# Kernel tuning notes

Measured on AMD Instinct MI355X. Metric: run time of the kernel, lower is better.

## Reference

```python
import jax, jax.numpy as jnp
import numpy as np

B, S, C, HD = 2, 4096, 2048, 128
H = C // HD  # 16 heads
EPS = 1.1920929e-07  # torch RMSNorm default eps for float32 (finfo.eps)


def _make_rope(seq_len, head_dim):
    # Standard RoPE 2x2 rotation matrices: [1, S, 1, head_dim//2, 2, 2]
    half = head_dim // 2
    freqs = 1.0 / (10000.0 ** (np.arange(0, half, dtype=np.float32) / half))
    ang = np.arange(seq_len, dtype=np.float32)[:, None] * freqs[None, :]  # [S, half]
    cos, sin = np.cos(ang), np.sin(ang)
    rot = np.stack([np.stack([cos, -sin], axis=-1),
                    np.stack([sin, cos], axis=-1)], axis=-2)  # [S, half, 2, 2]
    return jnp.asarray(rot[None, :, None])  # [1, S, 1, half, 2, 2]


def setup_inputs() -> dict:
    key = jax.random.key(0)
    ks = jax.random.split(key, 9)
    sc = 1.0 / np.sqrt(C)
    return {
        "x": jax.random.normal(ks[0], (B, S, C), jnp.float32),
        "rope": _make_rope(S, HD),
        "wq": jax.random.normal(ks[1], (C, C), jnp.float32) * sc,
        "bq": jax.random.normal(ks[2], (C,), jnp.float32) * 0.01,
        "wk": jax.random.normal(ks[3], (C, C), jnp.float32) * sc,
        "bk": jax.random.normal(ks[4], (C,), jnp.float32) * 0.01,
        "wv": jax.random.normal(ks[5], (C, C), jnp.float32) * sc,
        "bv": jax.random.normal(ks[6], (C,), jnp.float32) * 0.01,
        "q_norm_w": jnp.ones((HD,), jnp.float32),
        "k_norm_w": jnp.ones((HD,), jnp.float32),
    }


def _rmsnorm(t, w):
    t32 = t.astype(jnp.float32)
    inv = jax.lax.rsqrt(jnp.mean(t32 * t32, axis=-1, keepdims=True) + EPS)
    return (t32 * inv * w).astype(t.dtype)


def _apply_rotary(t, rope):
    # t: [B, S, H, HD] -> pairs [B, S, H, HD//2, 1, 2]; rope: [1, S, 1, HD//2, 2, 2]
    t32 = t.reshape(*t.shape[:-1], HD // 2, 1, 2).astype(jnp.float32)
    out = (rope * t32).sum(axis=-1)  # [B, S, H, HD//2, 2]
    return out.reshape(t.shape).astype(t.dtype)


def reference(x, rope, wq, bq, wk, bk, wv, bv, q_norm_w, k_norm_w):
    # QKV projections (torch Linear: x @ W^T + b)
    q = (jnp.einsum('bsc,oc->bso', x, wq) + bq).reshape(B, S, H, HD)
    k = (jnp.einsum('bsc,oc->bso', x, wk) + bk).reshape(B, S, H, HD)
    v = (jnp.einsum('bsc,oc->bso', x, wv) + bv).reshape(B, S, H, HD)
    # Per-head RMSNorm on q, k (in float32, cast back), then rotary
    q = _apply_rotary(_rmsnorm(q, q_norm_w), rope)
    k = _apply_rotary(_rmsnorm(k, k_norm_w), rope)
    return (q, k, v)
```

## Files before the change

kernel.cpp:

```cpp
#include <hip/hip_runtime.h>


#define M_DIM 8192
#define N_DIM 6144
#define K_DIM 2048
#define NKT 32
#define EPS_RMS 1.1920929e-07f

typedef __bf16 bf16x8 __attribute__((ext_vector_type(8)));
typedef float f32x4 __attribute__((ext_vector_type(4)));

__device__ __forceinline__ void gload16(const void* g, void* l) {
  __builtin_amdgcn_global_load_lds(
      (const __attribute__((address_space(1))) unsigned int*)g,
      (__attribute__((address_space(3))) unsigned int*)l, 16, 0, 0);
}

__device__ __forceinline__ unsigned short f2bf(float f) {
  union { float f; unsigned u; } x; x.f = f;
  unsigned r = x.u + 0x7FFFu + ((x.u >> 16) & 1u);
  return (unsigned short)(r >> 16);
}

__global__ void __launch_bounds__(256) cvt_kernel(const float* __restrict__ s,
                                                  unsigned short* __restrict__ d, int n4) {
  int i = blockIdx.x * blockDim.x + threadIdx.x;
  const int stride = gridDim.x * blockDim.x;
  for (; i < n4; i += stride) {
    const float4 v = reinterpret_cast<const float4*>(s)[i];
    ushort4 o;
    o.x = f2bf(v.x); o.y = f2bf(v.y); o.z = f2bf(v.z); o.w = f2bf(v.w);
    reinterpret_cast<ushort4*>(d)[i] = o;
  }
}

#define LDS4(ARR, BASE, OFF) (*(const f32x4*)((const char*)(ARR) + (BASE) + (OFF)))

#define MFMA_PH(MH, NH)                                                              \
  {                                                                                  \
    _Pragma("unroll")                                                                \
    for (int mf4 = 0; mf4 < 4; ++mf4) {                                              \
      _Pragma("unroll")                                                              \
      for (int nf2 = 0; nf2 < 2; ++nf2) {                                            \
        f32x4& c = acc[(MH) * 4 + mf4][(NH) * 2 + nf2];                              \
        c = __builtin_amdgcn_mfma_f32_16x16x32_bf16(                                 \
            __builtin_bit_cast(bf16x8, Af[mf4][0]),                                  \
            __builtin_bit_cast(bf16x8, Bf[NH][nf2][0]), c, 0, 0, 0);                 \
        c = __builtin_amdgcn_mfma_f32_16x16x32_bf16(                                 \
            __builtin_bit_cast(bf16x8, Af[mf4][1]),                                  \
            __builtin_bit_cast(bf16x8, Bf[NH][nf2][1]), c, 0, 0, 0);                 \
      }                                                                              \
    }                                                                                \
  }

__global__ void __launch_bounds__(512, 2) gemm_fused(
    const unsigned short* __restrict__ xbf, const unsigned short* __restrict__ wbf,
    const float* __restrict__ rope,
    const float* __restrict__ bq, const float* __restrict__ bk, const float* __restrict__ bv,
    const float* __restrict__ qnw, const float* __restrict__ knw,
    float* __restrict__ dout) {
  const int id = blockIdx.x;
  const int sw = (id & 7) * 96 + (id >> 3);
  const int bm = sw / 24;
  const int bn = sw - bm * 24;
  const int m0 = bm << 8, n0 = bn << 8;
  const int tid = threadIdx.x;
  const int w = tid >> 6, l = tid & 63;
  const int l15 = l & 15, lhi = l >> 4;
  const int wr = w >> 2, wc = w & 3;

  __shared__ __align__(16) unsigned short As[32768];
  __shared__ __align__(16) unsigned short Bs[32768];

  const int srow = tid >> 3;
  const int schunk = (tid & 7) ^ (srow & 7);
  const unsigned short* aSrc = xbf + ((size_t)(m0 + srow) << 11) + (schunk << 3);
  const unsigned short* bSrc = wbf + ((size_t)(n0 + srow) << 11) + (schunk << 3);
  char* aDst = (char*)As + (w << 10);
  char* bDst = (char*)Bs + (w << 10);

#define STA(KT, Q) gload16(aSrc + ((size_t)(Q) << 17) + ((KT) << 6), aDst + ((((KT) & 1) << 15) + ((Q) << 13)))
#define STB(KT, Q) gload16(bSrc + ((size_t)(Q) << 17) + ((KT) << 6), bDst + ((((KT) & 1) << 15) + ((Q) << 13)))

  const int sl0 = ((lhi ^ (l15 & 7)) << 4);
  const int sl1 = (((lhi + 4) ^ (l15 & 7)) << 4);
  unsigned a0 = (wr << 14) + (l15 << 7) + sl0;
  unsigned a1 = (wr << 14) + (l15 << 7) + sl1;
  unsigned b0 = (wc << 13) + (l15 << 7) + sl0;
  unsigned b1 = (wc << 13) + (l15 << 7) + sl1;

  f32x4 acc[8][4];
#pragma unroll
  for (int i = 0; i < 8; ++i)
#pragma unroll
    for (int j = 0; j < 4; ++j) acc[i][j] = (f32x4){0.f, 0.f, 0.f, 0.f};

  f32x4 Af[4][2];
  f32x4 Bf[2][2][2];

  STA(0, 0); STA(0, 2);
  STB(0, 0); STB(0, 1); STB(0, 2); STB(0, 3);
  STA(0, 1); STA(0, 3);
  asm volatile("s_waitcnt vmcnt(2)" ::: "memory");
  __builtin_amdgcn_s_barrier();
  asm volatile("" ::: "memory");

  for (int kt = 0; kt < NKT; ++kt) {
    const bool notLast = (kt < NKT - 1);
    Af[0][0] = LDS4(As, a0, 0);    Af[1][0] = LDS4(As, a0, 2048);
    Af[2][0] = LDS4(As, a0, 4096); Af[3][0] = LDS4(As, a0, 6144);
    Af[0][1] = LDS4(As, a1, 0);    Af[1][1] = LDS4(As, a1, 2048);
    Af[2][1] = LDS4(As, a1, 4096); Af[3][1] = LDS4(As, a1, 6144);
    Bf[0][0][0] = LDS4(Bs, b0, 0);    Bf[0][1][0] = LDS4(Bs, b0, 2048);
    Bf[0][0][1] = LDS4(Bs, b1, 0);    Bf[0][1][1] = LDS4(Bs, b1, 2048);
    Bf[1][0][0] = LDS4(Bs, b0, 4096); Bf[1][1][0] = LDS4(Bs, b0, 6144);
    Bf[1][0][1] = LDS4(Bs, b1, 4096); Bf[1][1][1] = LDS4(Bs, b1, 6144);
    if (notLast) {
      STA(kt + 1, 0); STA(kt + 1, 2);
      STB(kt + 1, 0); STB(kt + 1, 1); STB(kt + 1, 2); STB(kt + 1, 3);
    }
    __builtin_amdgcn_s_setprio(1);
    MFMA_PH(0, 0);
    MFMA_PH(0, 1);
    __builtin_amdgcn_s_setprio(0);
    if (notLast) { asm volatile("s_waitcnt vmcnt(6)" ::: "memory"); }
    else         { asm volatile("s_waitcnt vmcnt(0)" ::: "memory"); }
    __builtin_amdgcn_s_barrier();
    asm volatile("" ::: "memory");
    Af[0][0] = LDS4(As, a0, 8192);  Af[1][0] = LDS4(As, a0, 10240);
    Af[2][0] = LDS4(As, a0, 12288); Af[3][0] = LDS4(As, a0, 14336);
    Af[0][1] = LDS4(As, a1, 8192);  Af[1][1] = LDS4(As, a1, 10240);
    Af[2][1] = LDS4(As, a1, 12288); Af[3][1] = LDS4(As, a1, 14336);
    if (notLast) { STA(kt + 1, 1); STA(kt + 1, 3); }
    __builtin_amdgcn_s_setprio(1);
    MFMA_PH(1, 0);
    MFMA_PH(1, 1);
    __builtin_amdgcn_s_setprio(0);
    if (notLast) { asm volatile("s_waitcnt vmcnt(2)" ::: "memory"); }
    __builtin_amdgcn_s_barrier();
    asm volatile("" ::: "memory");
    a0 ^= 32768u; a1 ^= 32768u; b0 ^= 32768u; b1 ^= 32768u;
  }

  float* scr = (float*)As;
  const int sec = bn >> 3;
  const int nsec = (n0 & 2047) + (wc << 6);
  const float* bias = sec == 0 ? bq : (sec == 1 ? bk : bv);
  float biasv[4];
#pragma unroll
  for (int nf = 0; nf < 4; ++nf) biasv[nf] = bias[nsec + nf * 16 + l15];
  const size_t outBase = ((size_t)sec << 24);

  if (sec < 2) {
    const float* nwp = sec ? knw : qnw;
    const int colh = (wc & 1) << 6;
    float nwv[4];
#pragma unroll
    for (int nf = 0; nf < 4; ++nf) nwv[nf] = nwp[colh + nf * 16 + l15];
    float ssv[8][4];
#pragma unroll
    for (int mf = 0; mf < 8; ++mf) {
#pragma unroll
      for (int j = 0; j < 4; ++j) {
        float ss = 0.f;
#pragma unroll
        for (int nf = 0; nf < 4; ++nf) {
          const float t = acc[mf][nf][j] + biasv[nf];
          ss += t * t;
        }
        ss += __shfl_xor(ss, 1);
        ss += __shfl_xor(ss, 2);
        ss += __shfl_xor(ss, 4);
        ss += __shfl_xor(ss, 8);
        ssv[mf][j] = ss;
      }
    }
    if (l15 == 0) {
#pragma unroll
      for (int mf = 0; mf < 8; ++mf)
#pragma unroll
        for (int j = 0; j < 4; ++j)
          scr[(w << 7) + mf * 16 + (lhi << 2) + j] = ssv[mf][j];
    }
    __syncthreads();
#pragma unroll
    for (int mf = 0; mf < 8; ++mf) {
#pragma unroll
      for (int j = 0; j < 4; ++j) {
        const float tot = ssv[mf][j] + scr[((w ^ 1) << 7) + mf * 16 + (lhi << 2) + j];
        const float inv = rsqrtf(tot * (1.0f / 128.0f) + EPS_RMS);
        const int m = m0 + (wr << 7) + mf * 16 + (lhi << 2) + j;
        const float* rp = rope + ((size_t)(m & 4095) << 8);
        float* orow = dout + outBase + ((size_t)m << 11) + nsec + l15;
#pragma unroll
        for (int nf = 0; nf < 4; ++nf) {
          const float tn = (acc[mf][nf][j] + biasv[nf]) * inv * nwv[nf];
          const float pn = __shfl_xor(tn, 1);
          const int ch = colh + nf * 16 + l15;
          const int jr = ch >> 1;
          const float o = fmaf(rp[jr << 2], tn, rp[(jr << 2) + 1 + (ch & 1)] * pn);
          orow[nf << 4] = o;
        }
      }
    }
  } else {
#pragma unroll
    for (int mf = 0; mf < 8; ++mf)
#pragma unroll
      for (int j = 0; j < 4; ++j) {
        const int m = m0 + (wr << 7) + mf * 16 + (lhi << 2) + j;
        float* orow = dout + outBase + ((size_t)m << 11) + nsec + l15;
#pragma unroll
        for (int nf = 0; nf < 4; ++nf) orow[nf << 4] = acc[mf][nf][j] + biasv[nf];
      }
  }
}

extern "C" void kernel_launch(void* const* d_in, const int* in_sizes, int n_in,
                              void* d_out, int out_size, void* d_ws, size_t ws_size,
                              hipStream_t stream) {
  const float* x = (const float*)d_in[0];
  const float* rope = (const float*)d_in[1];
  const float* wq = (const float*)d_in[2];
  const float* bq = (const float*)d_in[3];
  const float* wk = (const float*)d_in[4];
  const float* bk = (const float*)d_in[5];
  const float* wv = (const float*)d_in[6];
  const float* bv = (const float*)d_in[7];
  const float* qnw = (const float*)d_in[8];
  const float* knw = (const float*)d_in[9];

  unsigned short* xbf = (unsigned short*)d_ws;
  unsigned short* wbf = xbf + (size_t)M_DIM * K_DIM;

  cvt_kernel<<<2048, 256, 0, stream>>>(x, xbf, M_DIM * K_DIM / 4);
  cvt_kernel<<<1024, 256, 0, stream>>>(wq, wbf, K_DIM * K_DIM / 4);
  cvt_kernel<<<1024, 256, 0, stream>>>(wk, wbf + (size_t)K_DIM * K_DIM, K_DIM * K_DIM / 4);
  cvt_kernel<<<1024, 256, 0, stream>>>(wv, wbf + (size_t)2 * K_DIM * K_DIM, K_DIM * K_DIM / 4);

  gemm_fused<<<(M_DIM / 256) * (N_DIM / 256), 512, 0, stream>>>(
      xbf, wbf, rope, bq, bk, bv, qnw, knw, (float*)d_out);
}
```

Baseline: 261.2 us.

## Interleave LDS reads with MFMAs via sched_group_barrier and remap tile order per XCD

Reorders the LDS fragment loads so the operands for the first MFMAs arrive first, and adds sched_group_barrier hints that interleave ds_read groups with MFMA groups in both half-iterations. This is meant to hide LDS latency behind matrix math instead of issuing every read up front. It also changes the block-to-tile mapping so each XCD owns 4 contiguous M-tiles across all N-tiles, which changes L2 reuse patterns. The scheduling constraints could raise register pressure or serialize issue if the group counts do not match the real instruction stream.

```diff
diff --git a/kernel.cpp b/kernel.cpp
--- a/kernel.cpp
+++ b/kernel.cpp
@@ -35,6 +35,9 @@
 }
 
 #define LDS4(ARR, BASE, OFF) (*(const f32x4*)((const char*)(ARR) + (BASE) + (OFF)))
+
+#define SGB_DS(N)   __builtin_amdgcn_sched_group_barrier(0x100, (N), 0)
+#define SGB_MFMA(N) __builtin_amdgcn_sched_group_barrier(0x8, (N), 0)
 
 #define MFMA_PH(MH, NH)                                                              \
   {                                                                                  \
@@ -60,9 +63,10 @@
     const float* __restrict__ qnw, const float* __restrict__ knw,
     float* __restrict__ dout) {
   const int id = blockIdx.x;
-  const int sw = (id & 7) * 96 + (id >> 3);
-  const int bm = sw / 24;
-  const int bn = sw - bm * 24;
+  const int xcd = id & 7;
+  const int j = id >> 3;
+  const int bm = (xcd << 2) | (j & 3);
+  const int bn = j >> 2;
   const int m0 = bm << 8, n0 = bn << 8;
   const int tid = threadIdx.x;
   const int w = tid >> 6, l = tid & 63;
@@ -93,7 +97,7 @@
 #pragma unroll
   for (int i = 0; i < 8; ++i)
 #pragma unroll
-    for (int j = 0; j < 4; ++j) acc[i][j] = (f32x4){0.f, 0.f, 0.f, 0.f};
+    for (int jj = 0; jj < 4; ++jj) acc[i][jj] = (f32x4){0.f, 0.f, 0.f, 0.f};
 
   f32x4 Af[4][2];
   f32x4 Bf[2][2][2];
@@ -107,14 +111,14 @@
 
   for (int kt = 0; kt < NKT; ++kt) {
     const bool notLast = (kt < NKT - 1);
-    Af[0][0] = LDS4(As, a0, 0);    Af[1][0] = LDS4(As, a0, 2048);
-    Af[2][0] = LDS4(As, a0, 4096); Af[3][0] = LDS4(As, a0, 6144);
-    Af[0][1] = LDS4(As, a1, 0);    Af[1][1] = LDS4(As, a1, 2048);
-    Af[2][1] = LDS4(As, a1, 4096); Af[3][1] = LDS4(As, a1, 6144);
-    Bf[0][0][0] = LDS4(Bs, b0, 0);    Bf[0][1][0] = LDS4(Bs, b0, 2048);
-    Bf[0][0][1] = LDS4(Bs, b1, 0);    Bf[0][1][1] = LDS4(Bs, b1, 2048);
-    Bf[1][0][0] = LDS4(Bs, b0, 4096); Bf[1][1][0] = LDS4(Bs, b0, 6144);
-    Bf[1][0][1] = LDS4(Bs, b1, 4096); Bf[1][1][1] = LDS4(Bs, b1, 6144);
+    Af[0][0] = LDS4(As, a0, 0);        Af[0][1] = LDS4(As, a1, 0);
+    Bf[0][0][0] = LDS4(Bs, b0, 0);     Bf[0][0][1] = LDS4(Bs, b1, 0);
+    Bf[0][1][0] = LDS4(Bs, b0, 2048);  Bf[0][1][1] = LDS4(Bs, b1, 2048);
+    Af[1][0] = LDS4(As, a0, 2048);     Af[1][1] = LDS4(As, a1, 2048);
+    Af[2][0] = LDS4(As, a0, 4096);     Af[2][1] = LDS4(As, a1, 4096);
+    Af[3][0] = LDS4(As, a0, 6144);     Af[3][1] = LDS4(As, a1, 6144);
+    Bf[1][0][0] = LDS4(Bs, b0, 4096);  Bf[1][0][1] = LDS4(Bs, b1, 4096);
+    Bf[1][1][0] = LDS4(Bs, b0, 6144);  Bf[1][1][1] = LDS4(Bs, b1, 6144);
     if (notLast) {
       STA(kt + 1, 0); STA(kt + 1, 2);
       STB(kt + 1, 0); STB(kt + 1, 1); STB(kt + 1, 2); STB(kt + 1, 3);
@@ -122,19 +126,30 @@
     __builtin_amdgcn_s_setprio(1);
     MFMA_PH(0, 0);
     MFMA_PH(0, 1);
+    SGB_DS(4);  SGB_MFMA(2);
+    SGB_DS(2);  SGB_MFMA(2);
+    SGB_DS(2);  SGB_MFMA(4);
+    SGB_DS(2);  SGB_MFMA(4);
+    SGB_DS(2);  SGB_MFMA(4);
+    SGB_DS(4);  SGB_MFMA(16);
     __builtin_amdgcn_s_setprio(0);
     if (notLast) { asm volatile("s_waitcnt vmcnt(6)" ::: "memory"); }
     else         { asm volatile("s_waitcnt vmcnt(0)" ::: "memory"); }
     __builtin_amdgcn_s_barrier();
     asm volatile("" ::: "memory");
-    Af[0][0] = LDS4(As, a0, 8192);  Af[1][0] = LDS4(As, a0, 10240);
-    Af[2][0] = LDS4(As, a0, 12288); Af[3][0] = LDS4(As, a0, 14336);
-    Af[0][1] = LDS4(As, a1, 8192);  Af[1][1] = LDS4(As, a1, 10240);
-    Af[2][1] = LDS4(As, a1, 12288); Af[3][1] = LDS4(As, a1, 14336);
+    Af[0][0] = LDS4(As, a0, 8192);  Af[0][1] = LDS4(As, a1, 8192);
+    Af[1][0] = LDS4(As, a0, 10240); Af[1][1] = LDS4(As, a1, 10240);
+    Af[2][0] = LDS4(As, a0, 12288); Af[2][1] = LDS4(As, a1, 12288);
+    Af[3][0] = LDS4(As, a0, 14336); Af[3][1] = LDS4(As, a1, 14336);
     if (notLast) { STA(kt + 1, 1); STA(kt + 1, 3); }
     __builtin_amdgcn_s_setprio(1);
     MFMA_PH(1, 0);
     MFMA_PH(1, 1);
+    SGB_DS(2);  SGB_MFMA(4);
+    SGB_DS(2);  SGB_MFMA(4);
+    SGB_DS(2);  SGB_MFMA(4);
+    SGB_DS(2);  SGB_MFMA(4);
+    SGB_MFMA(16);
     __builtin_amdgcn_s_setprio(0);
     if (notLast) { asm volatile("s_waitcnt vmcnt(2)" ::: "memory"); }
     __builtin_amdgcn_s_barrier();
@@ -161,40 +176,40 @@
 #pragma unroll
     for (int mf = 0; mf < 8; ++mf) {
 #pragma unroll
-      for (int j = 0; j < 4; ++j) {
+      for (int jj = 0; jj < 4; ++jj) {
         float ss = 0.f;
 #pragma unroll
         for (int nf = 0; nf < 4; ++nf) {
-          const float t = acc[mf][nf][j] + biasv[nf];
+          const float t = acc[mf][nf][jj] + biasv[nf];
           ss += t * t;
         }
         ss += __shfl_xor(ss, 1);
         ss += __shfl_xor(ss, 2);
         ss += __shfl_xor(ss, 4);
         ss += __shfl_xor(ss, 8);
-        ssv[mf][j] = ss;
+        ssv[mf][jj] = ss;
       }
     }
     if (l15 == 0) {
 #pragma unroll
       for (int mf = 0; mf < 8; ++mf)
 #pragma unroll
-        for (int j = 0; j < 4; ++j)
-          scr[(w << 7) + mf * 16 + (lhi << 2) + j] = ssv[mf][j];
+        for (int jj = 0; jj < 4; ++jj)
+          scr[(w << 7) + mf * 16 + (lhi << 2) + jj] = ssv[mf][jj];
     }
     __syncthreads();
 #pragma unroll
     for (int mf = 0; mf < 8; ++mf) {
 #pragma unroll
-      for (int j = 0; j < 4; ++j) {
-        const float tot = ssv[mf][j] + scr[((w ^ 1) << 7) + mf * 16 + (lhi << 2) + j];
+      for (int jj = 0; jj < 4; ++jj) {
+        const float tot = ssv[mf][jj] + scr[((w ^ 1) << 7) + mf * 16 + (lhi << 2) + jj];
         const float inv = rsqrtf(tot * (1.0f / 128.0f) + EPS_RMS);
-        const int m = m0 + (wr << 7) + mf * 16 + (lhi << 2) + j;
+        const int m = m0 + (wr << 7) + mf * 16 + (lhi << 2) + jj;
         const float* rp = rope + ((size_t)(m & 4095) << 8);
         float* orow = dout + outBase + ((size_t)m << 11) + nsec + l15;
 #pragma unroll
         for (int nf = 0; nf < 4; ++nf) {
-          const float tn = (acc[mf][nf][j] + biasv[nf]) * inv * nwv[nf];
+          const float tn = (acc[mf][nf][jj] + biasv[nf]) * inv * nwv[nf];
           const float pn = __shfl_xor(tn, 1);
           const int ch = colh + nf * 16 + l15;
           const int jr = ch >> 1;
@@ -207,11 +222,11 @@
 #pragma unroll
     for (int mf = 0; mf < 8; ++mf)
 #pragma unroll
-      for (int j = 0; j < 4; ++j) {
-        const int m = m0 + (wr << 7) + mf * 16 + (lhi << 2) + j;
+      for (int jj = 0; jj < 4; ++jj) {
+        const int m = m0 + (wr << 7) + mf * 16 + (lhi << 2) + jj;
         float* orow = dout + outBase + ((size_t)m << 11) + nsec + l15;
 #pragma unroll
-        for (int nf = 0; nf < 4; ++nf) orow[nf << 4] = acc[mf][nf][j] + biasv[nf];
+        for (int nf = 0; nf < 4; ++nf) orow[nf << 4] = acc[mf][nf][jj] + biasv[nf];
       }
   }
 }
```

Result: faster. 240.3 us (-8.0%).
